# Optimization experiments

Measured on AMD Instinct MI355X. Metric: run time of the kernel, lower is better.

The kernel has to match this reference:

```python
import jax, jax.numpy as jnp
import numpy as np

B, S, D, H = 64, 197, 768, 12
HD = D // H  # 64
WIN = 14
NUM_REL = (2 * WIN - 1) ** 2 + 3  # 732


def _build_rel_index():
    ch = np.arange(WIN)
    coords = np.stack(np.meshgrid(ch, ch, indexing='ij'))  # [2, W, W]
    flat = coords.reshape(2, -1)  # [2, W*W]
    rel = flat[:, :, None] - flat[:, None, :]  # [2, W*W, W*W]
    rel = rel.transpose(1, 2, 0).astype(np.int64)
    rel[:, :, 0] += WIN - 1
    rel[:, :, 1] += WIN - 1
    rel[:, :, 0] *= 2 * WIN - 1
    idx = np.zeros((WIN * WIN + 1, WIN * WIN + 1), dtype=np.int64)
    idx[1:, 1:] = rel.sum(-1)
    idx[0, :] = NUM_REL - 3
    idx[:, 0] = NUM_REL - 2
    idx[0, 0] = NUM_REL - 1
    return idx


def setup_inputs() -> dict:
    key = jax.random.key(0)
    ks = jax.random.split(key, 7)
    s = 0.02
    return {
        'hidden_states': jax.random.normal(ks[0], (B, S, D), jnp.float32),
        'wq': jax.random.normal(ks[1], (D, D), jnp.float32) * s,
        'bq': jax.random.normal(ks[2], (D,), jnp.float32) * s,
        'wk': jax.random.normal(ks[3], (D, D), jnp.float32) * s,  # key has no bias in BEiT
        'wv': jax.random.normal(ks[4], (D, D), jnp.float32) * s,
        'bv': jax.random.normal(ks[5], (D,), jnp.float32) * s,
        'bias_table': jax.random.normal(ks[6], (NUM_REL, H), jnp.float32) * s,
        'rel_index': jnp.asarray(_build_rel_index(), jnp.int32),
    }


def reference(hidden_states, wq, bq, wk, wv, bv, bias_table, rel_index):
    def heads(x):  # [B,S,D] -> [B,H,S,HD]
        return x.reshape(B, S, H, HD).transpose(0, 2, 1, 3)

    q = heads(hidden_states @ wq.T + bq)
    k = heads(hidden_states @ wk.T)
    v = heads(hidden_states @ wv.T + bv)

    scale = 1.0 / jnp.sqrt(jnp.asarray(HD, hidden_states.dtype))
    scores = jnp.einsum('bhqd,bhkd->bhqk', q, k) * scale  # [B,H,S,S]

    # relative position bias: [S,S,H] -> [1,H,S,S]
    rel_bias = bias_table[rel_index].transpose(2, 0, 1)[None]
    scores = scores + rel_bias

    probs = jax.nn.softmax(scores, axis=-1)
    ctx = jnp.einsum('bhqk,bhkd->bhqd', probs, v)  # [B,H,S,HD]
    return ctx.transpose(0, 2, 1, 3).reshape(B, S, D)
```

## Files before the change

kernel.cpp:

```cpp
#include <hip/hip_runtime.h>


#define S_LEN 197
#define HEADS 12
#define HDIM 64
#define DMODEL 768
#define BATCH 64
#define MROWS (BATCH * S_LEN)
#define MPAD 12672
#define NCOLS (3 * DMODEL)
#define KDIM DMODEL
#define NQT 13

typedef __attribute__((ext_vector_type(8))) short short8;
typedef __attribute__((ext_vector_type(4))) float floatx4;

#define GLD16(gp, lp)                                                                  \
  __builtin_amdgcn_global_load_lds(                                                    \
      (const __attribute__((address_space(1))) unsigned int*)(gp),                     \
      (__attribute__((address_space(3))) unsigned int*)(lp), 16, 0, 0)

__device__ __forceinline__ ushort f2bf(float f) {
  union { float f; unsigned int i; } x;
  x.f = f;
  unsigned int r = x.i + 0x7fffu + ((x.i >> 16) & 1u);
  return (ushort)(r >> 16);
}

__global__ void k_convert_h(const float* __restrict__ hs, ushort* __restrict__ hbf) {
  int col = blockIdx.x * 256 + threadIdx.x;
  int row = blockIdx.y;
  float v = (row < MROWS) ? hs[(size_t)row * DMODEL + col] : 0.f;
  hbf[(size_t)row * DMODEL + col] = f2bf(v);
}

__global__ void k_convert_w(const float* __restrict__ wq, const float* __restrict__ wk,
                            const float* __restrict__ wv, ushort* __restrict__ wbf) {
  int col = blockIdx.x * 256 + threadIdx.x;
  int row = blockIdx.y;
  const float* src = (row < DMODEL) ? &wq[(size_t)row * DMODEL]
                     : (row < 2 * DMODEL) ? &wk[(size_t)(row - DMODEL) * DMODEL]
                                          : &wv[(size_t)(row - 2 * DMODEL) * DMODEL];
  wbf[(size_t)row * DMODEL + col] = f2bf(src[col]);
}

__global__ void k_bias_expand(const float* __restrict__ bt, const int* __restrict__ ridx,
                              float* __restrict__ biasF) {
  int idx = blockIdx.x * 256 + threadIdx.x;
  if (idx >= HEADS * NQT * NQT * 64) return;
  int lane = idx & 63;
  int rest = idx >> 6;
  int t = rest % NQT;
  int rest2 = rest / NQT;
  int qt = rest2 % NQT;
  int h = rest2 / NQT;
  int l16 = lane & 15, quad = lane >> 4;
  int q = qt * 16 + l16;
#pragma unroll
  for (int r = 0; r < 4; ++r) {
    int key = t * 16 + quad * 4 + r;
    float v = -1e30f;
    if (q < S_LEN && key < S_LEN) v = bt[ridx[q * S_LEN + key] * HEADS + h];
    biasF[(size_t)idx * 4 + r] = v;
  }
}

__global__ __launch_bounds__(256) void k_gemm_qkv(
    const ushort* __restrict__ A, const ushort* __restrict__ W,
    const float* __restrict__ bq, const float* __restrict__ bv,
    ushort* __restrict__ Cb) {
  __shared__ __align__(16) ushort SH[128 * 128];
  ushort* As = SH;
  ushort* Bs = SH + 128 * 32;
  int tid = threadIdx.x;
  int wave = tid >> 6, lane = tid & 63;
  int quad = lane >> 4, l16 = lane & 15;
  int m0 = blockIdx.y * 128, n0 = blockIdx.x * 128;
  int wm = (wave & 1) * 64, wn = (wave >> 1) * 64;
  int swz = (quad ^ (l16 & 3)) << 3;

  floatx4 acc[4][4];
  floatx4 z = {0.f, 0.f, 0.f, 0.f};
#pragma unroll
  for (int i = 0; i < 4; ++i)
#pragma unroll
    for (int j = 0; j < 4; ++j) acc[i][j] = z;

  int p0 = wave * 128 + lane;
  for (int kb = 0; kb < KDIM; kb += 32) {
    const ushort* Arow = A + (size_t)m0 * KDIM + kb;
    const ushort* Brow = W + (size_t)n0 * KDIM + kb;
#pragma unroll
    for (int s = 0; s < 2; ++s) {
      int p = p0 + s * 64;
      int r = p >> 2;
      int kc = ((p ^ r) & 3) << 3;
      GLD16(&Arow[(size_t)r * KDIM + kc], &As[p * 8]);
      GLD16(&Brow[(size_t)r * KDIM + kc], &Bs[p * 8]);
    }
    __syncthreads();
    short8 af[4], bfr[4];
#pragma unroll
    for (int i = 0; i < 4; ++i) {
      af[i] = *(const short8*)(&As[(wm + i * 16 + l16) * 32 + swz]);
      bfr[i] = *(const short8*)(&Bs[(wn + i * 16 + l16) * 32 + swz]);
    }
#pragma unroll
    for (int i = 0; i < 4; ++i)
#pragma unroll
      for (int j = 0; j < 4; ++j)
        acc[i][j] = __builtin_amdgcn_mfma_f32_16x16x32_bf16(af[i], bfr[j], acc[i][j], 0, 0, 0);
    __syncthreads();
  }

#pragma unroll
  for (int j = 0; j < 4; ++j) {
    int coln = wn + j * 16 + l16;
    int col = n0 + coln;
    float bias = (col < DMODEL) ? bq[col] : ((col >= 2 * DMODEL) ? bv[col - 2 * DMODEL] : 0.f);
    float scl = (col < DMODEL) ? 0.125f : 1.0f;
#pragma unroll
    for (int i = 0; i < 4; ++i)
#pragma unroll
      for (int r = 0; r < 4; ++r) {
        int row = wm + i * 16 + quad * 4 + r;
        int ch = (coln >> 3) ^ (row & 7);
        SH[row * 128 + (ch << 3) + (coln & 7)] = f2bf((acc[i][j][r] + bias) * scl);
      }
  }
  __syncthreads();
#pragma unroll
  for (int p = 0; p < 2; ++p) {
    int row = p * 64 + wave * 16 + (lane >> 2);
    int q4 = lane & 3;
    ushort* gC = Cb + (size_t)(m0 + row) * NCOLS + n0;
#pragma unroll
    for (int c = 0; c < 4; ++c) {
      int cp = c * 4 + q4;
      int ch = cp ^ (row & 7);
      *(uint4*)&gC[cp * 8] = *(const uint4*)&SH[row * 128 + (ch << 3)];
    }
  }
}

__global__ __launch_bounds__(256) void k_attn_mfma(
    const ushort* __restrict__ Cb0, const float* __restrict__ biasF,
    float* __restrict__ out) {
  __shared__ __align__(16) ushort Vt[HDIM * 256];
  int bh = blockIdx.x;
  int b = bh / HEADS, h = bh - b * HEADS;
  int tid = threadIdx.x;
  int wave = tid >> 6, lane = tid & 63;
  int quad = lane >> 4, l16 = lane & 15;
  const ushort* Cb = Cb0 + (size_t)b * S_LEN * NCOLS;
  const int qoff = h * HDIM, koff = DMODEL + h * HDIM, voff = 2 * DMODEL + h * HDIM;

  {
    uint4 z4 = {0u, 0u, 0u, 0u};
    for (int i = tid; i < HDIM * 256 / 8; i += 256) ((uint4*)Vt)[i] = z4;
  }
  __syncthreads();
  for (int idx = tid; idx < S_LEN * 32; idx += 256) {
    int key = idx >> 5, dp = (idx & 31) * 2;
    unsigned int v = *(const unsigned int*)&Cb[(size_t)key * NCOLS + voff + dp];
    int ch = key >> 3, co = key & 7;
    Vt[dp * 256 + ((ch ^ (dp & 7)) << 3) + co] = (ushort)(v & 0xffffu);
    Vt[(dp + 1) * 256 + ((ch ^ ((dp + 1) & 7)) << 3) + co] = (ushort)(v >> 16);
  }
  __syncthreads();

  for (int qt = wave; qt < NQT; qt += 4) {
    int q0 = qt * 16;
    int q = q0 + l16;
    short8 qb0 = *(const short8*)&Cb[(size_t)q * NCOLS + qoff + quad * 8];
    short8 qb1 = *(const short8*)&Cb[(size_t)q * NCOLS + qoff + 32 + quad * 8];
    const float* bF = biasF + ((size_t)((h * NQT + qt) * NQT) * 64 + lane) * 4;

    floatx4 sacc[NQT];
#pragma unroll
    for (int t = 0; t < NQT; ++t) {
      floatx4 cin = *(const floatx4*)&bF[t * 256];
      short8 ka0 = *(const short8*)&Cb[(size_t)(t * 16 + l16) * NCOLS + koff + quad * 8];
      short8 ka1 = *(const short8*)&Cb[(size_t)(t * 16 + l16) * NCOLS + koff + 32 + quad * 8];
      floatx4 s1 = __builtin_amdgcn_mfma_f32_16x16x32_bf16(ka0, qb0, cin, 0, 0, 0);
      sacc[t] = __builtin_amdgcn_mfma_f32_16x16x32_bf16(ka1, qb1, s1, 0, 0, 0);
    }

    float mx = -3e38f;
#pragma unroll
    for (int t = 0; t < NQT; ++t)
#pragma unroll
      for (int r = 0; r < 4; ++r) mx = fmaxf(mx, sacc[t][r]);
    mx = fmaxf(mx, __shfl_xor(mx, 16));
    mx = fmaxf(mx, __shfl_xor(mx, 32));
    float sum = 0.f;
    unsigned int pbf[NQT][2];
#pragma unroll
    for (int t = 0; t < NQT; ++t) {
      float e0 = __expf(sacc[t][0] - mx), e1 = __expf(sacc[t][1] - mx);
      float e2 = __expf(sacc[t][2] - mx), e3 = __expf(sacc[t][3] - mx);
      sum += (e0 + e1) + (e2 + e3);
      union { float f; unsigned int u; } a, bb, c, d;
      a.f = e0; bb.f = e1; c.f = e2; d.f = e3;
      pbf[t][0] = ((a.u + 0x8000u) >> 16) | ((bb.u + 0x8000u) & 0xffff0000u);
      pbf[t][1] = ((c.u + 0x8000u) >> 16) | ((d.u + 0x8000u) & 0xffff0000u);
    }
    sum += __shfl_xor(sum, 16);
    sum += __shfl_xor(sum, 32);
    float inv = 1.f / sum;

    floatx4 oacc[4];
    floatx4 zz = {0.f, 0.f, 0.f, 0.f};
#pragma unroll
    for (int dt = 0; dt < 4; ++dt) oacc[dt] = zz;
    int sel0 = ((quad & 1) * 2) * 16 + l16;
    int sel1 = sel0 + 16;
#pragma unroll
    for (int kk = 0; kk < 7; ++kk) {
      unsigned int u0 = 0, u1 = 0, u2 = 0, u3 = 0;
#pragma unroll
      for (int half = 0; half < 2; ++half) {
        int t = 2 * kk + half;
        if (t < NQT) {
          unsigned int v0 = __shfl((int)pbf[t][0], sel0);
          unsigned int v1 = __shfl((int)pbf[t][1], sel0);
          unsigned int v2 = __shfl((int)pbf[t][0], sel1);
          unsigned int v3 = __shfl((int)pbf[t][1], sel1);
          if ((quad >> 1) == half) { u0 = v0; u1 = v1; u2 = v2; u3 = v3; }
        }
      }
      union { uint4 u; short8 s; } pf;
      pf.u.x = u0; pf.u.y = u1; pf.u.z = u2; pf.u.w = u3;
#pragma unroll
      for (int dt = 0; dt < 4; ++dt) {
        int d = dt * 16 + l16;
        short8 vf = *(const short8*)&Vt[d * 256 + (((kk * 4 + quad) ^ (d & 7)) << 3)];
        oacc[dt] = __builtin_amdgcn_mfma_f32_16x16x32_bf16(vf, pf.s, oacc[dt], 0, 0, 0);
      }
    }

    if (q < S_LEN) {
      float* og = out + ((size_t)b * S_LEN + q) * DMODEL + h * HDIM + quad * 4;
#pragma unroll
      for (int dt = 0; dt < 4; ++dt) {
        floatx4 o = oacc[dt];
        float4 st = make_float4(o[0] * inv, o[1] * inv, o[2] * inv, o[3] * inv);
        *(float4*)&og[dt * 16] = st;
      }
    }
  }
}

extern "C" void kernel_launch(void* const* d_in, const int* in_sizes, int n_in,
                              void* d_out, int out_size, void* d_ws, size_t ws_size,
                              hipStream_t stream) {
  const float* hs = (const float*)d_in[0];
  const float* wq = (const float*)d_in[1];
  const float* bq = (const float*)d_in[2];
  const float* wk = (const float*)d_in[3];
  const float* wv = (const float*)d_in[4];
  const float* bv = (const float*)d_in[5];
  const float* bt = (const float*)d_in[6];
  const int* ridx = (const int*)d_in[7];
  float* out = (float*)d_out;

  ushort* hbf = (ushort*)d_ws;
  ushort* wbf = hbf + (size_t)MPAD * KDIM;
  ushort* Cb = wbf + (size_t)NCOLS * KDIM;
  float* biasF = (float*)(Cb + (size_t)MPAD * NCOLS);

  k_convert_h<<<dim3(3, MPAD), 256, 0, stream>>>(hs, hbf);
  k_convert_w<<<dim3(3, NCOLS), 256, 0, stream>>>(wq, wk, wv, wbf);
  int nbias = (HEADS * NQT * NQT * 64 + 255) / 256;
  k_bias_expand<<<nbias, 256, 0, stream>>>(bt, ridx, biasF);
  k_gemm_qkv<<<dim3(NCOLS / 128, MPAD / 128), 256, 0, stream>>>(hbf, wbf, bq, bv, Cb);
  k_attn_mfma<<<BATCH * HEADS, 256, 0, stream>>>(Cb, biasF, out);
}
```

Baseline: 253.5 us.

## Fuse prep kernels, remap GEMM tiles for XCD locality, fix swizzle, stage K in LDS

Three conversion and bias kernels are merged into one grid-stride prep kernel with 8-wide vectorized stores, which saves launches. The QKV GEMM remaps block indices so that groups of 222 consecutive tiles land on the same XCD for better L2 reuse, and it changes the LDS swizzle pattern to reduce bank conflicts. The attention kernel now stages K fragments in LDS once per block instead of having every wave reload them from global memory. The cost is extra LDS use, which may lower occupancy.

Result: faster. 237.6 us (-6.3%).

```diff
diff --git a/kernel.cpp b/kernel.cpp
--- a/kernel.cpp
+++ b/kernel.cpp
@@ -11,6 +11,8 @@
 #define NCOLS (3 * DMODEL)
 #define KDIM DMODEL
 #define NQT 13
+#define NTILE (NCOLS / 128)
+#define MTILE (MPAD / 128)
 
 typedef __attribute__((ext_vector_type(8))) short short8;
 typedef __attribute__((ext_vector_type(4))) float floatx4;
@@ -27,41 +29,57 @@
   return (ushort)(r >> 16);
 }
 
-__global__ void k_convert_h(const float* __restrict__ hs, ushort* __restrict__ hbf) {
-  int col = blockIdx.x * 256 + threadIdx.x;
-  int row = blockIdx.y;
-  float v = (row < MROWS) ? hs[(size_t)row * DMODEL + col] : 0.f;
-  hbf[(size_t)row * DMODEL + col] = f2bf(v);
-}
-
-__global__ void k_convert_w(const float* __restrict__ wq, const float* __restrict__ wk,
-                            const float* __restrict__ wv, ushort* __restrict__ wbf) {
-  int col = blockIdx.x * 256 + threadIdx.x;
-  int row = blockIdx.y;
-  const float* src = (row < DMODEL) ? &wq[(size_t)row * DMODEL]
-                     : (row < 2 * DMODEL) ? &wk[(size_t)(row - DMODEL) * DMODEL]
-                                          : &wv[(size_t)(row - 2 * DMODEL) * DMODEL];
-  wbf[(size_t)row * DMODEL + col] = f2bf(src[col]);
-}
-
-__global__ void k_bias_expand(const float* __restrict__ bt, const int* __restrict__ ridx,
-                              float* __restrict__ biasF) {
-  int idx = blockIdx.x * 256 + threadIdx.x;
-  if (idx >= HEADS * NQT * NQT * 64) return;
-  int lane = idx & 63;
-  int rest = idx >> 6;
-  int t = rest % NQT;
-  int rest2 = rest / NQT;
-  int qt = rest2 % NQT;
-  int h = rest2 / NQT;
-  int l16 = lane & 15, quad = lane >> 4;
-  int q = qt * 16 + l16;
-#pragma unroll
-  for (int r = 0; r < 4; ++r) {
-    int key = t * 16 + quad * 4 + r;
-    float v = -1e30f;
-    if (q < S_LEN && key < S_LEN) v = bt[ridx[q * S_LEN + key] * HEADS + h];
-    biasF[(size_t)idx * 4 + r] = v;
+__global__ __launch_bounds__(256) void k_prep(
+    const float* __restrict__ hs, const float* __restrict__ wq,
+    const float* __restrict__ wk, const float* __restrict__ wv,
+    const float* __restrict__ bt, const int* __restrict__ ridx,
+    ushort* __restrict__ hbf, ushort* __restrict__ wbf, float* __restrict__ biasF) {
+  int gid = blockIdx.x * 256 + threadIdx.x;
+  int gsz = gridDim.x * 256;
+  for (int i = gid; i < MPAD * KDIM / 8; i += gsz) {
+    int base = i * 8;
+    int row = base / KDIM;
+    ushort o[8];
+    if (row < MROWS) {
+      const float* s = hs + (size_t)base;
+#pragma unroll
+      for (int e = 0; e < 8; ++e) o[e] = f2bf(s[e]);
+    } else {
+#pragma unroll
+      for (int e = 0; e < 8; ++e) o[e] = 0;
+    }
+    *(uint4*)&hbf[base] = *(const uint4*)o;
+  }
+  for (int i = gid; i < NCOLS * KDIM / 8; i += gsz) {
+    int base = i * 8;
+    int row = base / KDIM;
+    int col = base - row * KDIM;
+    const float* src = (row < DMODEL) ? &wq[(size_t)row * KDIM]
+                       : (row < 2 * DMODEL) ? &wk[(size_t)(row - DMODEL) * KDIM]
+                                            : &wv[(size_t)(row - 2 * DMODEL) * KDIM];
+    ushort o[8];
+#pragma unroll
+    for (int e = 0; e < 8; ++e) o[e] = f2bf(src[col + e]);
+    *(uint4*)&wbf[base] = *(const uint4*)o;
+  }
+  for (int idx = gid; idx < HEADS * NQT * NQT * 64; idx += gsz) {
+    int lane = idx & 63;
+    int rest = idx >> 6;
+    int t = rest % NQT;
+    int rest2 = rest / NQT;
+    int qt = rest2 % NQT;
+    int h = rest2 / NQT;
+    int l16 = lane & 15, quad = lane >> 4;
+    int q = qt * 16 + l16;
+    floatx4 v;
+#pragma unroll
+    for (int r = 0; r < 4; ++r) {
+      int key = t * 16 + quad * 4 + r;
+      float x = -1e30f;
+      if (q < S_LEN && key < S_LEN) x = bt[ridx[q * S_LEN + key] * HEADS + h];
+      v[r] = x;
+    }
+    *(floatx4*)&biasF[(size_t)idx * 4] = v;
   }
 }
 
@@ -75,9 +93,20 @@
   int tid = threadIdx.x;
   int wave = tid >> 6, lane = tid & 63;
   int quad = lane >> 4, l16 = lane & 15;
-  int m0 = blockIdx.y * 128, n0 = blockIdx.x * 128;
+
+  int linear = blockIdx.y * NTILE + blockIdx.x;
+  int m_t, n_t;
+  if (linear < 1776) {
+    int g = (linear & 7) * 222 + (linear >> 3);
+    m_t = g / NTILE;
+    n_t = g - m_t * NTILE;
+  } else {
+    m_t = linear / NTILE;
+    n_t = linear - m_t * NTILE;
+  }
+  int m0 = m_t * 128, n0 = n_t * 128;
   int wm = (wave & 1) * 64, wn = (wave >> 1) * 64;
-  int swz = (quad ^ (l16 & 3)) << 3;
+  int swz = (quad ^ ((l16 >> 1) & 3)) << 3;
 
   floatx4 acc[4][4];
   floatx4 z = {0.f, 0.f, 0.f, 0.f};
@@ -94,7 +123,7 @@
     for (int s = 0; s < 2; ++s) {
       int p = p0 + s * 64;
       int r = p >> 2;
-      int kc = ((p ^ r) & 3) << 3;
+      int kc = ((p & 3) ^ ((p >> 3) & 3)) << 3;
       GLD16(&Arow[(size_t)r * KDIM + kc], &As[p * 8]);
       GLD16(&Brow[(size_t)r * KDIM + kc], &Bs[p * 8]);
     }
@@ -147,6 +176,7 @@
     const ushort* __restrict__ Cb0, const float* __restrict__ biasF,
     float* __restrict__ out) {
   __shared__ __align__(16) ushort Vt[HDIM * 256];
+  __shared__ __align__(16) ushort Ka[NQT * 2 * 512];
   int bh = blockIdx.x;
   int b = bh / HEADS, h = bh - b * HEADS;
   int tid = threadIdx.x;
@@ -167,6 +197,11 @@
     Vt[dp * 256 + ((ch ^ (dp & 7)) << 3) + co] = (ushort)(v & 0xffffu);
     Vt[(dp + 1) * 256 + ((ch ^ ((dp + 1) & 7)) << 3) + co] = (ushort)(v >> 16);
   }
+  for (int th = wave; th < NQT * 2; th += 4) {
+    int t = th >> 1, half = th & 1;
+    short8 kf = *(const short8*)&Cb[(size_t)(t * 16 + l16) * NCOLS + koff + half * 32 + quad * 8];
+    *(short8*)&Ka[th * 512 + lane * 8] = kf;
+  }
   __syncthreads();
 
   for (int qt = wave; qt < NQT; qt += 4) {
@@ -180,8 +215,8 @@
 #pragma unroll
     for (int t = 0; t < NQT; ++t) {
       floatx4 cin = *(const floatx4*)&bF[t * 256];
-      short8 ka0 = *(const short8*)&Cb[(size_t)(t * 16 + l16) * NCOLS + koff + quad * 8];
-      short8 ka1 = *(const short8*)&Cb[(size_t)(t * 16 + l16) * NCOLS + koff + 32 + quad * 8];
+      short8 ka0 = *(const short8*)&Ka[(t * 2 + 0) * 512 + lane * 8];
+      short8 ka1 = *(const short8*)&Ka[(t * 2 + 1) * 512 + lane * 8];
       floatx4 s1 = __builtin_amdgcn_mfma_f32_16x16x32_bf16(ka0, qb0, cin, 0, 0, 0);
       sacc[t] = __builtin_amdgcn_mfma_f32_16x16x32_bf16(ka1, qb1, s1, 0, 0, 0);
     }
@@ -269,10 +304,7 @@
   ushort* Cb = wbf + (size_t)NCOLS * KDIM;
   float* biasF = (float*)(Cb + (size_t)MPAD * NCOLS);
 
-  k_convert_h<<<dim3(3, MPAD), 256, 0, stream>>>(hs, hbf);
-  k_convert_w<<<dim3(3, NCOLS), 256, 0, stream>>>(wq, wk, wv, wbf);
-  int nbias = (HEADS * NQT * NQT * 64 + 255) / 256;
-  k_bias_expand<<<nbias, 256, 0, stream>>>(bt, ridx, biasF);
-  k_gemm_qkv<<<dim3(NCOLS / 128, MPAD / 128), 256, 0, stream>>>(hbf, wbf, bq, bv, Cb);
+  k_prep<<<2048, 256, 0, stream>>>(hs, wq, wk, wv, bt, ridx, hbf, wbf, biasF);
+  k_gemm_qkv<<<dim3(NTILE, MTILE), 256, 0, stream>>>(hbf, wbf, bq, bv, Cb);
   k_attn_mfma<<<BATCH * HEADS, 256, 0, stream>>>(Cb, biasF, out);
 }
```
